# Optimization experiments

Measured on AMD Instinct MI355X. Metric: run time of the kernel, lower is better.

The kernel has to match this reference:

```python
import jax, jax.numpy as jnp
import numpy as np

# Faithful JAX port of kornia.filters.median_blur as used by MedianBlur in eval mode:
#  - zero padding to keep 'same' spatial size
#  - unfold kxk neighborhoods, take the (k*k)//2-th order statistic (k odd -> exact median,
#    matching torch.median's lower-median convention for odd counts)

def _median_blur(img, k):
    # img: [B, C, H, W]; k: odd python int
    pad = k // 2
    B, C, H, W = img.shape
    x = jnp.pad(img, ((0, 0), (0, 0), (pad, pad), (pad, pad)))  # zero pad (kornia default)
    # Stack the k*k shifted views -> [B, C, k*k, H, W] (fixed small loop over kernel taps)
    patches = jnp.stack(
        [x[:, :, i:i + H, j:j + W] for i in range(k) for j in range(k)], axis=2
    )
    med_idx = (k * k) // 2  # k odd -> unique middle element
    return jnp.sort(patches, axis=2)[:, :, med_idx]


def setup_inputs() -> dict:
    key = jax.random.key(0)
    img = jax.random.normal(key, (8, 3, 512, 512), dtype=jnp.float32)
    return {"img": img, "kernel_size": 5}


def reference(img, kernel_size):
    return _median_blur(img, int(kernel_size))
```

## Files before the change

### kernel.cpp

```cpp
#include <hip/hip_runtime.h>


__device__ __forceinline__ void cswap(float& a, float& b) {
    float lo = fminf(a, b);
    float hi = fmaxf(a, b);
    a = lo; b = hi;
}

#define SORT4 { cswap(v0,v1); cswap(v2,v3); cswap(v0,v2); cswap(v1,v3); cswap(v1,v2); }

#define COL_TOP2(a0,a1,a2,a3,a4,o3,o4) { \
    float v0=a0,v1=a1,v2=a2,v3=a3,v4=a4; SORT4; \
    cswap(v3,v4); cswap(v2,v3); (o3)=v3; (o4)=v4; (void)v0; (void)v1; }

#define COL_TOP3(a0,a1,a2,a3,a4,o2,o3,o4) { \
    float v0=a0,v1=a1,v2=a2,v3=a3,v4=a4; SORT4; \
    cswap(v3,v4); cswap(v2,v3); cswap(v1,v2); (o2)=v2; (o3)=v3; (o4)=v4; (void)v0; }

#define COL_MID3(a0,a1,a2,a3,a4,o1,o2,o3) { \
    float v0=a0,v1=a1,v2=a2,v3=a3,v4=a4; SORT4; \
    cswap(v3,v4); cswap(v2,v3); cswap(v1,v2); cswap(v0,v1); (o1)=v1; (o2)=v2; (o3)=v3; }

#define COL_BOT3(a0,a1,a2,a3,a4,o0,o1,o2) { \
    float v0=a0,v1=a1,v2=a2,v3=a3,v4=a4; SORT4; \
    cswap(v0,v4); cswap(v1,v4); cswap(v2,v4); (o0)=v0; (o1)=v1; (o2)=v2; (void)v3; }

#define COL_BOT2(a0,a1,a2,a3,a4,o0,o1) { \
    float v0=a0,v1=a1,v2=a2,v3=a3,v4=a4; SORT4; \
    cswap(v0,v4); cswap(v1,v4); (o0)=v0; (o1)=v1; (void)v2; (void)v3; }

__global__ __launch_bounds__(256) void median5_kernel(const float* __restrict__ img,
                                                      float* __restrict__ out)
{
    const int W = 512, H = 512;
    const int x  = blockIdx.x * 64 + threadIdx.x;
    const int ty = blockIdx.y * 4 + threadIdx.y;
    const int y0 = ty * 8;
    const int p  = blockIdx.z;

    const float* __restrict__ base = img + ((size_t)p << 18);
    float* __restrict__ obase = out + ((size_t)p << 18) + x;

    const int  cx0 = max(x - 2, 0), cx1 = max(x - 1, 0);
    const int  cx3 = min(x + 1, W - 1), cx4 = min(x + 2, W - 1);
    const bool m0 = (x - 2) >= 0, m1 = (x - 1) >= 0;
    const bool m3 = (x + 1) < W,  m4 = (x + 2) < W;

    float r[5][5];

#define LOAD_ROW(yy, S) do { \
    const int _y = (yy); \
    if ((unsigned)_y < (unsigned)H) { \
        const float* _rp = base + _y * W; \
        float v0 = _rp[cx0]; if (!m0) v0 = 0.f; \
        float v1 = _rp[cx1]; if (!m1) v1 = 0.f; \
        float v2 = _rp[x]; \
        float v3 = _rp[cx3]; if (!m3) v3 = 0.f; \
        float v4 = _rp[cx4]; if (!m4) v4 = 0.f; \
        SORT4; \
        cswap(v3,v4); cswap(v2,v3); cswap(v1,v2); cswap(v0,v1); \
        r[S][0]=v0; r[S][1]=v1; r[S][2]=v2; r[S][3]=v3; r[S][4]=v4; \
    } else { \
        r[S][0]=0.f; r[S][1]=0.f; r[S][2]=0.f; r[S][3]=0.f; r[S][4]=0.f; \
    } \
} while (0)

    LOAD_ROW(y0 - 2, 0);
    LOAD_ROW(y0 - 1, 1);
    LOAD_ROW(y0 + 0, 2);
    LOAD_ROW(y0 + 1, 3);

#define PROC(i, S0, S1, S2, S3, S4) do { \
    LOAD_ROW(y0 + (i) + 2, S4); \
    float b[13]; \
    COL_TOP2(r[S0][0], r[S1][0], r[S2][0], r[S3][0], r[S4][0], b[0], b[1]); \
    COL_TOP3(r[S0][1], r[S1][1], r[S2][1], r[S3][1], r[S4][1], b[2], b[3], b[4]); \
    COL_MID3(r[S0][2], r[S1][2], r[S2][2], r[S3][2], r[S4][2], b[5], b[6], b[7]); \
    COL_BOT3(r[S0][3], r[S1][3], r[S2][3], r[S3][3], r[S4][3], b[8], b[9], b[10]); \
    COL_BOT2(r[S0][4], r[S1][4], r[S2][4], r[S3][4], r[S4][4], b[11], b[12]); \
    float w[8]; \
    _Pragma("unroll") for (int k = 0; k < 8; ++k) w[k] = b[k]; \
     \
    _Pragma("unroll") for (int j = 1; j < 8; ++j) cswap(w[0], w[j]); \
    _Pragma("unroll") for (int j = 1; j < 7; ++j) cswap(w[j], w[7]); \
    w[0] = b[8]; \
     \
    _Pragma("unroll") for (int j = 1; j < 7; ++j) cswap(w[0], w[j]); \
    _Pragma("unroll") for (int j = 1; j < 6; ++j) cswap(w[j], w[6]); \
    w[0] = b[9]; \
     \
    _Pragma("unroll") for (int j = 1; j < 6; ++j) cswap(w[0], w[j]); \
    _Pragma("unroll") for (int j = 1; j < 5; ++j) cswap(w[j], w[5]); \
    w[0] = b[10]; \
     \
    _Pragma("unroll") for (int j = 1; j < 5; ++j) cswap(w[0], w[j]); \
    _Pragma("unroll") for (int j = 1; j < 4; ++j) cswap(w[j], w[4]); \
    w[0] = b[11]; \
     \
    _Pragma("unroll") for (int j = 1; j < 4; ++j) cswap(w[0], w[j]); \
    _Pragma("unroll") for (int j = 1; j < 3; ++j) cswap(w[j], w[3]); \
    w[0] = b[12]; \
     \
    float mn = fminf(w[0], w[1]); \
    float mx = fmaxf(w[0], w[1]); \
    obase[(y0 + (i)) * W] = fmaxf(mn, fminf(mx, w[2])); \
} while (0)

    PROC(0, 0, 1, 2, 3, 4);
    PROC(1, 1, 2, 3, 4, 0);
    PROC(2, 2, 3, 4, 0, 1);
    PROC(3, 3, 4, 0, 1, 2);
    PROC(4, 4, 0, 1, 2, 3);
    PROC(5, 0, 1, 2, 3, 4);
    PROC(6, 1, 2, 3, 4, 0);
    PROC(7, 2, 3, 4, 0, 1);
}

extern "C" void kernel_launch(void* const* d_in, const int* in_sizes, int n_in,
                              void* d_out, int out_size, void* d_ws, size_t ws_size,
                              hipStream_t stream)
{
    const float* img = (const float*)d_in[0];
    float* out = (float*)d_out;

    dim3 block(64, 4, 1);
    dim3 grid(512 / 64, 512 / 8 / 4, 24);
    median5_kernel<<<grid, block, 0, stream>>>(img, out);
}
```

Measured before the change: 108.4 us.

## Replace forgetful median selection with merge-based selection network

```diff
diff --git a/kernel.cpp b/kernel.cpp
--- a/kernel.cpp
+++ b/kernel.cpp
@@ -9,9 +9,21 @@
 
 #define SORT4 { cswap(v0,v1); cswap(v2,v3); cswap(v0,v2); cswap(v1,v3); cswap(v1,v2); }
 
-#define COL_TOP2(a0,a1,a2,a3,a4,o3,o4) { \
-    float v0=a0,v1=a1,v2=a2,v3=a3,v4=a4; SORT4; \
-    cswap(v3,v4); cswap(v2,v3); (o3)=v3; (o4)=v4; (void)v0; (void)v1; }
+#define COL_TOP2(x0,x1,x2,x3,x4,o3,o4) { \
+    float lo01=fminf(x0,x1), hi01=fmaxf(x0,x1); \
+    float lo23=fminf(x2,x3), hi23=fmaxf(x2,x3); \
+    float mx4 = fmaxf(hi01,hi23); \
+    float s4  = fmaxf(fminf(hi01,hi23), fmaxf(lo01,lo23)); \
+    float hi  = fmaxf(mx4, x4), lo = fminf(mx4, x4); \
+    (o4) = hi; (o3) = fmaxf(s4, lo); }
+
+#define COL_BOT2(x0,x1,x2,x3,x4,o0,o1) { \
+    float lo01=fminf(x0,x1), hi01=fmaxf(x0,x1); \
+    float lo23=fminf(x2,x3), hi23=fmaxf(x2,x3); \
+    float mn4 = fminf(lo01,lo23); \
+    float s4  = fminf(fmaxf(lo01,lo23), fminf(hi01,hi23)); \
+    float lo  = fminf(mn4, x4), hi = fmaxf(mn4, x4); \
+    (o0) = lo; (o1) = fminf(s4, hi); }
 
 #define COL_TOP3(a0,a1,a2,a3,a4,o2,o3,o4) { \
     float v0=a0,v1=a1,v2=a2,v3=a3,v4=a4; SORT4; \
@@ -25,9 +37,11 @@
     float v0=a0,v1=a1,v2=a2,v3=a3,v4=a4; SORT4; \
     cswap(v0,v4); cswap(v1,v4); cswap(v2,v4); (o0)=v0; (o1)=v1; (o2)=v2; (void)v3; }
 
-#define COL_BOT2(a0,a1,a2,a3,a4,o0,o1) { \
-    float v0=a0,v1=a1,v2=a2,v3=a3,v4=a4; SORT4; \
-    cswap(v0,v4); cswap(v1,v4); (o0)=v0; (o1)=v1; (void)v2; (void)v3; }
+#define MERGE23(a0,a1,p0,p1,p2,L0,L1,L2,L3,L4) { \
+    float e0 = fminf(a0,p0), t = fmaxf(a0,p0); \
+    float e1 = fminf(t,p2),  e2 = fmaxf(t,p2); \
+    float o0 = fminf(a1,p1), o1 = fmaxf(a1,p1); \
+    (L0)=e0; (L1)=fminf(o0,e1); (L2)=fmaxf(o0,e1); (L3)=fminf(o1,e2); (L4)=fmaxf(o1,e2); }
 
 __global__ __launch_bounds__(256) void median5_kernel(const float* __restrict__ img,
                                                       float* __restrict__ out)
@@ -43,25 +57,25 @@
 
     const int  cx0 = max(x - 2, 0), cx1 = max(x - 1, 0);
     const int  cx3 = min(x + 1, W - 1), cx4 = min(x + 2, W - 1);
-    const bool m0 = (x - 2) >= 0, m1 = (x - 1) >= 0;
-    const bool m3 = (x + 1) < W,  m4 = (x + 2) < W;
+    const bool m0v = (x - 2) >= 0, m1v = (x - 1) >= 0;
+    const bool m3v = (x + 1) < W,  m4v = (x + 2) < W;
 
     float r[5][5];
 
-#define LOAD_ROW(yy, S) do { \
+#define LOAD_ROW(yy, SL) do { \
     const int _y = (yy); \
     if ((unsigned)_y < (unsigned)H) { \
         const float* _rp = base + _y * W; \
-        float v0 = _rp[cx0]; if (!m0) v0 = 0.f; \
-        float v1 = _rp[cx1]; if (!m1) v1 = 0.f; \
+        float v0 = _rp[cx0]; if (!m0v) v0 = 0.f; \
+        float v1 = _rp[cx1]; if (!m1v) v1 = 0.f; \
         float v2 = _rp[x]; \
-        float v3 = _rp[cx3]; if (!m3) v3 = 0.f; \
-        float v4 = _rp[cx4]; if (!m4) v4 = 0.f; \
+        float v3 = _rp[cx3]; if (!m3v) v3 = 0.f; \
+        float v4 = _rp[cx4]; if (!m4v) v4 = 0.f; \
         SORT4; \
         cswap(v3,v4); cswap(v2,v3); cswap(v1,v2); cswap(v0,v1); \
-        r[S][0]=v0; r[S][1]=v1; r[S][2]=v2; r[S][3]=v3; r[S][4]=v4; \
+        r[SL][0]=v0; r[SL][1]=v1; r[SL][2]=v2; r[SL][3]=v3; r[SL][4]=v4; \
     } else { \
-        r[S][0]=0.f; r[S][1]=0.f; r[S][2]=0.f; r[S][3]=0.f; r[S][4]=0.f; \
+        r[SL][0]=0.f; r[SL][1]=0.f; r[SL][2]=0.f; r[SL][3]=0.f; r[SL][4]=0.f; \
     } \
 } while (0)
 
@@ -70,40 +84,30 @@
     LOAD_ROW(y0 + 0, 2);
     LOAD_ROW(y0 + 1, 3);
 
-#define PROC(i, S0, S1, S2, S3, S4) do { \
-    LOAD_ROW(y0 + (i) + 2, S4); \
-    float b[13]; \
-    COL_TOP2(r[S0][0], r[S1][0], r[S2][0], r[S3][0], r[S4][0], b[0], b[1]); \
-    COL_TOP3(r[S0][1], r[S1][1], r[S2][1], r[S3][1], r[S4][1], b[2], b[3], b[4]); \
-    COL_MID3(r[S0][2], r[S1][2], r[S2][2], r[S3][2], r[S4][2], b[5], b[6], b[7]); \
-    COL_BOT3(r[S0][3], r[S1][3], r[S2][3], r[S3][3], r[S4][3], b[8], b[9], b[10]); \
-    COL_BOT2(r[S0][4], r[S1][4], r[S2][4], r[S3][4], r[S4][4], b[11], b[12]); \
-    float w[8]; \
-    _Pragma("unroll") for (int k = 0; k < 8; ++k) w[k] = b[k]; \
+#define PROC(i, RA, RB, RC, RD, RE) do { \
+    LOAD_ROW(y0 + (i) + 2, RE); \
+    float a0,a1, p0,p1,p2, mm0,mm1,mm2, q0,q1,q2, d0,d1; \
+    COL_TOP2(r[RA][0], r[RB][0], r[RC][0], r[RD][0], r[RE][0], a0, a1); \
+    COL_TOP3(r[RA][1], r[RB][1], r[RC][1], r[RD][1], r[RE][1], p0, p1, p2); \
+    COL_MID3(r[RA][2], r[RB][2], r[RC][2], r[RD][2], r[RE][2], mm0, mm1, mm2); \
+    COL_BOT3(r[RA][3], r[RB][3], r[RC][3], r[RD][3], r[RE][3], q0, q1, q2); \
+    COL_BOT2(r[RA][4], r[RB][4], r[RC][4], r[RD][4], r[RE][4], d0, d1); \
+    float L0,L1,L2,L3,L4, R0,R1,R2,R3,R4; \
+    MERGE23(a0, a1, p0, p1, p2, L0, L1, L2, L3, L4); \
+    MERGE23(d0, d1, q0, q1, q2, R0, R1, R2, R3, R4); \
      \
-    _Pragma("unroll") for (int j = 1; j < 8; ++j) cswap(w[0], w[j]); \
-    _Pragma("unroll") for (int j = 1; j < 7; ++j) cswap(w[j], w[7]); \
-    w[0] = b[8]; \
+    float u  = fmaxf(L1,R1), v  = fminf(L3,R3); \
+    float O1 = fminf(u,v),   O2 = fmaxf(u,v); \
+    float u2 = fmaxf(L0,R0), v2 = fminf(L4,R4); \
+    float F1 = fminf(u2,v2), F2 = fmaxf(u2,v2); \
+    float G0 = fminf(L2,R2), G1 = fmaxf(L2,R2); \
+    float E2 = fmaxf(G0,F1), E3 = fminf(G1,F2); \
+    float Sa = fminf(O1,E2), Sb = fmaxf(O1,E2); \
+    float Sc = fminf(O2,E3), Sd = fmaxf(O2,E3); \
      \
-    _Pragma("unroll") for (int j = 1; j < 7; ++j) cswap(w[0], w[j]); \
-    _Pragma("unroll") for (int j = 1; j < 6; ++j) cswap(w[j], w[6]); \
-    w[0] = b[9]; \
-     \
-    _Pragma("unroll") for (int j = 1; j < 6; ++j) cswap(w[0], w[j]); \
-    _Pragma("unroll") for (int j = 1; j < 5; ++j) cswap(w[j], w[5]); \
-    w[0] = b[10]; \
-     \
-    _Pragma("unroll") for (int j = 1; j < 5; ++j) cswap(w[0], w[j]); \
-    _Pragma("unroll") for (int j = 1; j < 4; ++j) cswap(w[j], w[4]); \
-    w[0] = b[11]; \
-     \
-    _Pragma("unroll") for (int j = 1; j < 4; ++j) cswap(w[0], w[j]); \
-    _Pragma("unroll") for (int j = 1; j < 3; ++j) cswap(w[j], w[3]); \
-    w[0] = b[12]; \
-     \
-    float mn = fminf(w[0], w[1]); \
-    float mx = fmaxf(w[0], w[1]); \
-    obase[(y0 + (i)) * W] = fmaxf(mn, fminf(mx, w[2])); \
+    float med = fminf( fminf(fmaxf(Sa,mm2), fmaxf(Sb,mm1)), \
+                       fminf(fmaxf(Sc,mm0), Sd) ); \
+    obase[(y0 + (i)) * W] = med; \
 } while (0)
 
     PROC(0, 0, 1, 2, 3, 4);
```

After: 100.1 us. -7.6%, faster.
